# Kernel tuning notes

Measured on AMD Instinct MI355X. Metric: run time of the kernel, lower is better.

The kernel has to match this reference:

```python
import jax, jax.numpy as jnp
import numpy as np

K_SIZE = 7  # matches init_kwargs k_size
EPS = 1e-7


def setup_inputs() -> dict:
    key = jax.random.key(0)
    x = jax.random.normal(key, (4, 64, 128, 128), dtype=jnp.float32)
    return {"x": x}


def reference(x):
    K = K_SIZE
    P = K // 2
    B, C, H, W = x.shape
    # zero-pad spatially, same as F.unfold(padding=K//2)
    xp = jnp.pad(x, ((0, 0), (0, 0), (P, P), (P, P)))
    # gather k*k shifted views -> (B, C, K*K, H, W); fixed small loop over window offsets
    patches = jnp.stack(
        [xp[:, :, i:i + H, j:j + W] for i in range(K) for j in range(K)], axis=2
    )
    # dot product of center pixel with each neighbor over channels -> (B, K*K, H, W)
    sim = jnp.sum(x[:, :, None, :, :] * patches, axis=1)
    norm_center = jnp.sqrt(jnp.sum(x * x, axis=1))[:, None]          # (B,1,H,W)
    norm_patches = jnp.sqrt(jnp.sum(patches * patches, axis=1))       # (B,K*K,H,W)
    sim = sim / (norm_center * norm_patches + EPS)
    sim = jax.nn.softmax(sim, axis=1)  # softmax over the K*K window dim
    return sim.reshape(B, K * K, H * W)
```

## Files before the change

### kernel.cpp

```cpp
#include <hip/hip_runtime.h>
#include <math.h>

#define KK 49
#define H 128
#define W 128
#define C 64
#define NB 4
#define EPS 1e-7f
#define PLANE (H * W)

#define TW 32
#define TH 2
#define HW2 38
#define HH2 8
#define NPOS (HW2 * HH2)
#define NP2 (2 * NPOS)
#define CADDR (3 * HW2 + 3)


typedef _Float16 h2_t __attribute__((ext_vector_type(2)));

__device__ __forceinline__ float fdot2(unsigned int a, unsigned int b, float c) {
    return __builtin_amdgcn_fdot2(__builtin_bit_cast(h2_t, a),
                                  __builtin_bit_cast(h2_t, b), c, false);
}
__device__ __forceinline__ unsigned int packh2(float a, float b) {
    return __builtin_bit_cast(unsigned int, __builtin_amdgcn_cvt_pkrtz(a, b));
}

template<int Q>
__device__ __forceinline__ void compute_q(const uint4* __restrict__ bp,
                                          float (&acc)[13]) {
    constexpr int NK = (Q == 3) ? 13 : 12;
    const uint4 c0 = bp[CADDR];
    const uint4 c1 = bp[NPOS + CADDR];
#pragma unroll
    for (int l = 0; l < NK; ++l) {
        const int k = Q * 12 + l;
        const int off = (k / 7) * HW2 + (k % 7);
        const uint4 n0 = bp[off];
        const uint4 n1 = bp[NPOS + off];
        acc[l] = fdot2(c0.x, n0.x, acc[l]);
        acc[l] = fdot2(c0.y, n0.y, acc[l]);
        acc[l] = fdot2(c0.z, n0.z, acc[l]);
        acc[l] = fdot2(c0.w, n0.w, acc[l]);
        acc[l] = fdot2(c1.x, n1.x, acc[l]);
        acc[l] = fdot2(c1.y, n1.y, acc[l]);
        acc[l] = fdot2(c1.z, n1.z, acc[l]);
        acc[l] = fdot2(c1.w, n1.w, acc[l]);
    }
}

template<int Q>
__device__ __forceinline__ void sim_and_max(const float* __restrict__ snb,
                                            float (&acc)[13], float& m) {
    constexpr int NK = (Q == 3) ? 13 : 12;
    const float nc = snb[CADDR];
#pragma unroll
    for (int l = 0; l < NK; ++l) {
        const int k = Q * 12 + l;
        const int off = (k / 7) * HW2 + (k % 7);
        const float nn = snb[off];
        const float sv = __fdividef(acc[l], nc * nn + EPS);
        acc[l] = sv;
        m = fmaxf(m, sv);
    }
}

template<int Q>
__device__ __forceinline__ void exp_and_sum(float (&acc)[13], float m, float& sum) {
    constexpr int NK = (Q == 3) ? 13 : 12;
#pragma unroll
    for (int l = 0; l < NK; ++l) {
        const float e = __expf(acc[l] - m);
        acc[l] = e;
        sum += e;
    }
}

template<int Q>
__device__ __forceinline__ void store_q(float* __restrict__ op,
                                        const float (&acc)[13], float inv) {
    constexpr int NK = (Q == 3) ? 13 : 12;
#pragma unroll
    for (int l = 0; l < NK; ++l)
        op[(size_t)l << 14] = acc[l] * inv;
}

#define DISPATCH_Q(stmt)                                      \
    do {                                                      \
        if (s2 == 0)      { constexpr int Q = 0; stmt; }      \
        else if (s2 == 1) { constexpr int Q = 1; stmt; }      \
        else if (s2 == 2) { constexpr int Q = 2; stmt; }      \
        else              { constexpr int Q = 3; stmt; }      \
    } while (0)

__global__ __launch_bounds__(256, 2) void rsa_kernel(const float* __restrict__ x,
                                                     float* __restrict__ out) {
    __shared__ uint4 sx[2][NP2];
    __shared__ float sn2[NP2];
    __shared__ float snf[NPOS];
    __shared__ float comb[4][TW * TH];

    const int tid = threadIdx.x;
    const int w   = tid & 31;
    const int r   = (tid >> 5) & 1;
    const int s2  = tid >> 6;
    const int w0  = blockIdx.x * TW;
    const int h0  = blockIdx.y * TH;
    const int b   = blockIdx.z;
    const float* __restrict__ xb = x + (size_t)b * C * PLANE;

    const int roww = r * HW2 + w;
    const uint4* const base4[2] = { &sx[0][0] + roww, &sx[1][0] + roww };

    int goff[3], pos[3], hh[3];
    bool act[3], inb[3];
#pragma unroll
    for (int j = 0; j < 3; ++j) {
        int i = tid + j * 256;
        act[j] = (i < NP2);
        int ii = act[j] ? i : 0;
        int g  = (ii >= NPOS) ? 1 : 0;
        int p  = ii - g * NPOS;
        int rr = p / HW2, cc = p - rr * HW2;
        int gh = h0 - 3 + rr, gw = w0 - 3 + cc;
        inb[j]  = (gh >= 0) && (gh < H) && (gw >= 0) && (gw < W);
        goff[j] = gh * W + gw;
        pos[j]  = ii;
        hh[j]   = g;
    }

    uint4 pu[3];
    float np[3] = {0.f, 0.f, 0.f};

    auto load_pass = [&](int t) {
#pragma unroll
        for (int j = 0; j < 3; ++j) {
            uint4 u = make_uint4(0u, 0u, 0u, 0u);
            if (act[j] && inb[j]) {
                const float* p = xb + (size_t)(t * 16 + hh[j] * 8) * PLANE + goff[j];
                const float f0 = p[0];
                const float f1 = p[PLANE];
                const float f2 = p[2 * PLANE];
                const float f3 = p[3 * PLANE];
                const float f4 = p[4 * PLANE];
                const float f5 = p[5 * PLANE];
                const float f6 = p[6 * PLANE];
                const float f7 = p[7 * PLANE];
                u.x = packh2(f0, f1);
                u.y = packh2(f2, f3);
                u.z = packh2(f4, f5);
                u.w = packh2(f6, f7);
            }
            pu[j] = u;
        }
    };

    auto write_pass = [&](int buf) {
#pragma unroll
        for (int j = 0; j < 3; ++j) {
            if (act[j]) {
                sx[buf][pos[j]] = pu[j];
                np[j] = fdot2(pu[j].x, pu[j].x, np[j]);
                np[j] = fdot2(pu[j].y, pu[j].y, np[j]);
                np[j] = fdot2(pu[j].z, pu[j].z, np[j]);
                np[j] = fdot2(pu[j].w, pu[j].w, np[j]);
            }
        }
    };

    float acc[13];
#pragma unroll
    for (int l = 0; l < 13; ++l) acc[l] = 0.f;

    load_pass(0);
    write_pass(0);
    __syncthreads();
#pragma unroll
    for (int t = 0; t < 4; ++t) {
        const int buf = t & 1;
        if (t < 3) load_pass(t + 1);
        DISPATCH_Q(compute_q<Q>(base4[buf], acc));
        if (t < 3) write_pass(buf ^ 1);
        __syncthreads();
    }

#pragma unroll
    for (int j = 0; j < 3; ++j)
        if (act[j]) sn2[pos[j]] = np[j];
    __syncthreads();
    for (int i = tid; i < NPOS; i += 256) snf[i] = sqrtf(sn2[i] + sn2[i + NPOS]);
    __syncthreads();

    const float* snb = &snf[0] + roww;
    float m = -1e30f;
    DISPATCH_Q(sim_and_max<Q>(snb, acc, m));

    const int pxi = r * TW + w;
    comb[s2][pxi] = m;
    __syncthreads();
    m = fmaxf(fmaxf(comb[0][pxi], comb[1][pxi]), fmaxf(comb[2][pxi], comb[3][pxi]));
    __syncthreads();

    float sum = 0.f;
    DISPATCH_Q(exp_and_sum<Q>(acc, m, sum));
    comb[s2][pxi] = sum;
    __syncthreads();
    sum = (comb[0][pxi] + comb[1][pxi]) + (comb[2][pxi] + comb[3][pxi]);
    const float inv = __fdividef(1.f, sum);

    float* op = out + (((size_t)b * KK + s2 * 12) << 14) + ((h0 + r) << 7) + (w0 + w);
    DISPATCH_Q(store_q<Q>(op, acc, inv));
}

extern "C" void kernel_launch(void* const* d_in, const int* in_sizes, int n_in,
                              void* d_out, int out_size, void* d_ws, size_t ws_size,
                              hipStream_t stream) {
    const float* x = (const float*)d_in[0];
    float* out = (float*)d_out;

    dim3 block(256, 1, 1);
    dim3 grid(W / TW, H / TH, NB);
    rsa_kernel<<<grid, block, 0, stream>>>(x, out);
}
```

Before: 81.33 us.

## Load all 64 channels into shared memory at once instead of double-buffered passes

Replaces the four-pass, double-buffered channel pipeline with one bulk load of all 64 channels (fp16-packed) into shared memory, followed by a single compute pass and one barrier. Each thread now handles one halo position across all 8 channel groups, computing its norm directly, which removes the separate norm-reduction stage and several barriers. Shared-memory use grows to about 39KB, which may limit occupancy. Global loads are no longer overlapped with the dot-product compute. The softmax reduction scratch now reuses the tile buffer, which needs an extra barrier.

```diff
diff --git a/kernel.cpp b/kernel.cpp
--- a/kernel.cpp
+++ b/kernel.cpp
@@ -14,7 +14,6 @@
 #define HW2 38
 #define HH2 8
 #define NPOS (HW2 * HH2)
-#define NP2 (2 * NPOS)
 #define CADDR (3 * HW2 + 3)
 
 
@@ -32,22 +31,21 @@
 __device__ __forceinline__ void compute_q(const uint4* __restrict__ bp,
                                           float (&acc)[13]) {
     constexpr int NK = (Q == 3) ? 13 : 12;
-    const uint4 c0 = bp[CADDR];
-    const uint4 c1 = bp[NPOS + CADDR];
+    uint4 c[8];
+#pragma unroll
+    for (int g = 0; g < 8; ++g) c[g] = bp[g * NPOS + CADDR];
 #pragma unroll
     for (int l = 0; l < NK; ++l) {
         const int k = Q * 12 + l;
         const int off = (k / 7) * HW2 + (k % 7);
-        const uint4 n0 = bp[off];
-        const uint4 n1 = bp[NPOS + off];
-        acc[l] = fdot2(c0.x, n0.x, acc[l]);
-        acc[l] = fdot2(c0.y, n0.y, acc[l]);
-        acc[l] = fdot2(c0.z, n0.z, acc[l]);
-        acc[l] = fdot2(c0.w, n0.w, acc[l]);
-        acc[l] = fdot2(c1.x, n1.x, acc[l]);
-        acc[l] = fdot2(c1.y, n1.y, acc[l]);
-        acc[l] = fdot2(c1.z, n1.z, acc[l]);
-        acc[l] = fdot2(c1.w, n1.w, acc[l]);
+#pragma unroll
+        for (int g = 0; g < 8; ++g) {
+            const uint4 n = bp[g * NPOS + off];
+            acc[l] = fdot2(c[g].x, n.x, acc[l]);
+            acc[l] = fdot2(c[g].y, n.y, acc[l]);
+            acc[l] = fdot2(c[g].z, n.z, acc[l]);
+            acc[l] = fdot2(c[g].w, n.w, acc[l]);
+        }
     }
 }
 
@@ -97,10 +95,10 @@
 
 __global__ __launch_bounds__(256, 2) void rsa_kernel(const float* __restrict__ x,
                                                      float* __restrict__ out) {
-    __shared__ uint4 sx[2][NP2];
-    __shared__ float sn2[NP2];
+    __shared__ uint4 sx[8 * NPOS];
     __shared__ float snf[NPOS];
-    __shared__ float comb[4][TW * TH];
+    float* const combM = (float*)sx;
+    float* const combS = (float*)sx + 256;
 
     const int tid = threadIdx.x;
     const int w   = tid & 31;
@@ -112,102 +110,70 @@
     const float* __restrict__ xb = x + (size_t)b * C * PLANE;
 
     const int roww = r * HW2 + w;
-    const uint4* const base4[2] = { &sx[0][0] + roww, &sx[1][0] + roww };
+    const uint4* const bp = &sx[0] + roww;
 
-    int goff[3], pos[3], hh[3];
-    bool act[3], inb[3];
 #pragma unroll
-    for (int j = 0; j < 3; ++j) {
-        int i = tid + j * 256;
-        act[j] = (i < NP2);
-        int ii = act[j] ? i : 0;
-        int g  = (ii >= NPOS) ? 1 : 0;
-        int p  = ii - g * NPOS;
-        int rr = p / HW2, cc = p - rr * HW2;
-        int gh = h0 - 3 + rr, gw = w0 - 3 + cc;
-        inb[j]  = (gh >= 0) && (gh < H) && (gw >= 0) && (gw < W);
-        goff[j] = gh * W + gw;
-        pos[j]  = ii;
-        hh[j]   = g;
+    for (int j = 0; j < 2; ++j) {
+        const int i = tid + j * 256;
+        if (i < NPOS) {
+            const int rr = i / HW2, cc = i - rr * HW2;
+            const int gh = h0 - 3 + rr, gw = w0 - 3 + cc;
+            float s = 0.f;
+            if (gh >= 0 && gh < H && gw >= 0 && gw < W) {
+                const float* p = xb + gh * W + gw;
+#pragma unroll
+                for (int g = 0; g < 8; ++g) {
+                    float f0 = p[(size_t)(g * 8 + 0) * PLANE];
+                    float f1 = p[(size_t)(g * 8 + 1) * PLANE];
+                    float f2 = p[(size_t)(g * 8 + 2) * PLANE];
+                    float f3 = p[(size_t)(g * 8 + 3) * PLANE];
+                    float f4 = p[(size_t)(g * 8 + 4) * PLANE];
+                    float f5 = p[(size_t)(g * 8 + 5) * PLANE];
+                    float f6 = p[(size_t)(g * 8 + 6) * PLANE];
+                    float f7 = p[(size_t)(g * 8 + 7) * PLANE];
+                    uint4 u;
+                    u.x = packh2(f0, f1);
+                    u.y = packh2(f2, f3);
+                    u.z = packh2(f4, f5);
+                    u.w = packh2(f6, f7);
+                    sx[g * NPOS + i] = u;
+                    s = fdot2(u.x, u.x, s);
+                    s = fdot2(u.y, u.y, s);
+                    s = fdot2(u.z, u.z, s);
+                    s = fdot2(u.w, u.w, s);
+                }
+            } else {
+                const uint4 z = make_uint4(0u, 0u, 0u, 0u);
+#pragma unroll
+                for (int g = 0; g < 8; ++g) sx[g * NPOS + i] = z;
+            }
+            snf[i] = sqrtf(s);
+        }
     }
-
-    uint4 pu[3];
-    float np[3] = {0.f, 0.f, 0.f};
-
-    auto load_pass = [&](int t) {
-#pragma unroll
-        for (int j = 0; j < 3; ++j) {
-            uint4 u = make_uint4(0u, 0u, 0u, 0u);
-            if (act[j] && inb[j]) {
-                const float* p = xb + (size_t)(t * 16 + hh[j] * 8) * PLANE + goff[j];
-                const float f0 = p[0];
-                const float f1 = p[PLANE];
-                const float f2 = p[2 * PLANE];
-                const float f3 = p[3 * PLANE];
-                const float f4 = p[4 * PLANE];
-                const float f5 = p[5 * PLANE];
-                const float f6 = p[6 * PLANE];
-                const float f7 = p[7 * PLANE];
-                u.x = packh2(f0, f1);
-                u.y = packh2(f2, f3);
-                u.z = packh2(f4, f5);
-                u.w = packh2(f6, f7);
-            }
-            pu[j] = u;
-        }
-    };
-
-    auto write_pass = [&](int buf) {
-#pragma unroll
-        for (int j = 0; j < 3; ++j) {
-            if (act[j]) {
-                sx[buf][pos[j]] = pu[j];
-                np[j] = fdot2(pu[j].x, pu[j].x, np[j]);
-                np[j] = fdot2(pu[j].y, pu[j].y, np[j]);
-                np[j] = fdot2(pu[j].z, pu[j].z, np[j]);
-                np[j] = fdot2(pu[j].w, pu[j].w, np[j]);
-            }
-        }
-    };
+    __syncthreads();
 
     float acc[13];
 #pragma unroll
     for (int l = 0; l < 13; ++l) acc[l] = 0.f;
-
-    load_pass(0);
-    write_pass(0);
-    __syncthreads();
-#pragma unroll
-    for (int t = 0; t < 4; ++t) {
-        const int buf = t & 1;
-        if (t < 3) load_pass(t + 1);
-        DISPATCH_Q(compute_q<Q>(base4[buf], acc));
-        if (t < 3) write_pass(buf ^ 1);
-        __syncthreads();
-    }
-
-#pragma unroll
-    for (int j = 0; j < 3; ++j)
-        if (act[j]) sn2[pos[j]] = np[j];
-    __syncthreads();
-    for (int i = tid; i < NPOS; i += 256) snf[i] = sqrtf(sn2[i] + sn2[i + NPOS]);
-    __syncthreads();
+    DISPATCH_Q(compute_q<Q>(bp, acc));
 
     const float* snb = &snf[0] + roww;
     float m = -1e30f;
     DISPATCH_Q(sim_and_max<Q>(snb, acc, m));
 
+    __syncthreads();
     const int pxi = r * TW + w;
-    comb[s2][pxi] = m;
+    combM[s2 * 64 + pxi] = m;
     __syncthreads();
-    m = fmaxf(fmaxf(comb[0][pxi], comb[1][pxi]), fmaxf(comb[2][pxi], comb[3][pxi]));
-    __syncthreads();
+    m = fmaxf(fmaxf(combM[0 * 64 + pxi], combM[1 * 64 + pxi]),
+              fmaxf(combM[2 * 64 + pxi], combM[3 * 64 + pxi]));
 
     float sum = 0.f;
     DISPATCH_Q(exp_and_sum<Q>(acc, m, sum));
-    comb[s2][pxi] = sum;
+    combS[s2 * 64 + pxi] = sum;
     __syncthreads();
-    sum = (comb[0][pxi] + comb[1][pxi]) + (comb[2][pxi] + comb[3][pxi]);
+    sum = (combS[0 * 64 + pxi] + combS[1 * 64 + pxi]) +
+          (combS[2 * 64 + pxi] + combS[3 * 64 + pxi]);
     const float inv = __fdividef(1.f, sum);
 
     float* op = out + (((size_t)b * KK + s2 * 12) << 14) + ((h0 + r) << 7) + (w0 + w);
```

Result: slower. 84.32 us (+3.7%).
